# Kernel optimization log

Measured on AMD Instinct MI355X. Metric: run time of the kernel, lower is better.

## Reference

```python
import jax, jax.numpy as jnp
import numpy as np

DIMS = [2048, 1024, 512, 256, 128, 64, 32, 16, 8, 4, 2]
IN_CH = [3, 8, 32, 64, 64, 64, 128, 256, 512, 512, 512]
FEAT = [8, 32, 64, 64, 64, 128, 256, 512, 512, 512, 1024]
B = 512
K = 16


def setup_inputs() -> dict:
    key = jax.random.key(0)
    keys = jax.random.split(key, 64)
    inp = {"x": jax.random.normal(keys[0], (B, 3, 2048), dtype=jnp.float32)}
    for i, d in enumerate(DIMS):
        inp[f"c{i}"] = jax.random.randint(keys[1 + i], (d,), 0, 3, dtype=jnp.int64)
    for i in range(11):
        cin, f = IN_CH[i], FEAT[i]
        inp[f"W{i+1}"] = jax.random.normal(keys[20 + 2 * i], (3 * f, cin), dtype=jnp.float32) / jnp.sqrt(jnp.float32(cin))
        inp[f"b{i+1}"] = jnp.zeros((3 * f,), dtype=jnp.float32)
    inp["Wfc"] = jax.random.normal(keys[60], (K, 1024), dtype=jnp.float32) / jnp.sqrt(jnp.float32(1024))
    inp["bfc"] = jnp.zeros((K,), dtype=jnp.float32)
    return inp


def _kdconv(x, W, b, sel, featdim, dim):
    # pointwise conv (kernel size 1) + relu: [B, in, dim] -> [B, 3*featdim, dim]
    y = jax.nn.relu(jnp.einsum('oi,bid->bod', W, x) + b[None, :, None])
    bsz = y.shape[0]
    # faithful to torch: view [B, featdim, 3*dim], then gather index d*3 + sel[d]
    y = y.reshape(bsz, featdim, 3 * dim)
    idx = sel + 3 * jnp.arange(dim, dtype=sel.dtype)
    y = jnp.take(y, idx, axis=2)                       # [B, featdim, dim]
    y = y.reshape(bsz, featdim, dim // 2, 2)
    return jnp.max(y, axis=-1)                          # [B, featdim, dim//2]


def reference(x, c0, c1, c2, c3, c4, c5, c6, c7, c8, c9, c10,
              W1, b1, W2, b2, W3, b3, W4, b4, W5, b5, W6, b6,
              W7, b7, W8, b8, W9, b9, W10, b10, W11, b11, Wfc, bfc):
    cs = [c0, c1, c2, c3, c4, c5, c6, c7, c8, c9, c10]
    Ws = [W1, W2, W3, W4, W5, W6, W7, W8, W9, W10, W11]
    bs = [b1, b2, b3, b4, b5, b6, b7, b8, b9, b10, b11]
    y = x
    for i in range(11):
        y = _kdconv(y, Ws[i], bs[i], cs[i], FEAT[i], DIMS[i])
    y = y.reshape(-1, 1024)
    logits = y @ Wfc.T + bfc
    return jax.nn.log_softmax(logits, axis=1)
```

## Files before the change

### kernel.cpp

```cpp
#include <hip/hip_runtime.h>
#include <cstdint>
#include <cmath>


typedef __attribute__((ext_vector_type(8))) short bhalf8;
typedef __attribute__((ext_vector_type(4))) float floatx4;

__device__ __forceinline__ unsigned short f2bf(float f) {
    uint32_t u = __float_as_uint(f);
    u += 0x7FFFu + ((u >> 16) & 1u);
    return (unsigned short)(u >> 16);
}
__device__ __forceinline__ float bf2f(unsigned short u) {
    return __uint_as_float(((uint32_t)u) << 16);
}

struct WPrep {
    const float* src[9];
    unsigned short* dst[9];
    int n4[9];
};

__global__ __launch_bounds__(256)
void l01_kernel(const float* __restrict__ x,
                const float* __restrict__ W0, const float* __restrict__ b0,
                const int* __restrict__ sel0,
                const float* __restrict__ W1, const float* __restrict__ b1,
                const int* __restrict__ sel1,
                unsigned short* __restrict__ out,
                WPrep wp, int nL1) {
    const int tid = threadIdx.x;

    if ((int)blockIdx.x >= nL1) {
        const int stride = (gridDim.x - nL1) * 256;
        const int g0 = (blockIdx.x - nL1) * 256 + tid;
        #pragma unroll
        for (int l = 0; l < 9; ++l) {
            const float4* s = reinterpret_cast<const float4*>(wp.src[l]);
            uint2* d = reinterpret_cast<uint2*>(wp.dst[l]);
            for (int i = g0; i < wp.n4[l]; i += stride) {
                const float4 v = s[i];
                uint2 o;
                o.x = (uint32_t)f2bf(v.x) | ((uint32_t)f2bf(v.y) << 16);
                o.y = (uint32_t)f2bf(v.z) | ((uint32_t)f2bf(v.w) << 16);
                d[i] = o;
            }
        }
        return;
    }

    __shared__ float W0s[24][3]; __shared__ float b0s[24];
    __shared__ float W1s[96][8]; __shared__ float b1s[96];
    if (tid < 24) {
        W0s[tid][0] = W0[tid * 3 + 0];
        W0s[tid][1] = W0[tid * 3 + 1];
        W0s[tid][2] = W0[tid * 3 + 2];
        b0s[tid] = b0[tid];
    }
    if (tid < 96) {
        #pragma unroll
        for (int k = 0; k < 8; ++k) W1s[tid][k] = W1[tid * 8 + k];
        b1s[tid] = b1[tid];
    }
    __syncthreads();

    const int gid = blockIdx.x * 256 + tid;
    const int b  = gid >> 9;
    const int j1 = gid & 511;
    const float* xb = x + (size_t)b * 3 * 2048;

    float cols[2][8];
    int q1v[2];
    #pragma unroll
    for (int pos1 = 0; pos1 < 2; ++pos1) {
        const int d1 = 2 * j1 + pos1;
        const int e1 = 3 * d1 + sel1[d1];
        const int q1 = (e1 >= 1024) + (e1 >= 2048);
        const int p1 = e1 - q1 * 1024;
        q1v[pos1] = q1;

        float xv[2][3]; int qq0[2];
        #pragma unroll
        for (int pos0 = 0; pos0 < 2; ++pos0) {
            const int d0 = 2 * p1 + pos0;
            const int e0 = 3 * d0 + sel0[d0];
            const int q0 = (e0 >= 2048) + (e0 >= 4096);
            const int p0 = e0 - q0 * 2048;
            qq0[pos0] = q0;
            xv[pos0][0] = xb[p0];
            xv[pos0][1] = xb[2048 + p0];
            xv[pos0][2] = xb[4096 + p0];
        }
        #pragma unroll
        for (int f = 0; f < 8; ++f) {
            const int r0 = 3 * f + qq0[0], r1 = 3 * f + qq0[1];
            const float v0 = b0s[r0] + W0s[r0][0]*xv[0][0] + W0s[r0][1]*xv[0][1] + W0s[r0][2]*xv[0][2];
            const float v1 = b0s[r1] + W0s[r1][0]*xv[1][0] + W0s[r1][1]*xv[1][1] + W0s[r1][2]*xv[1][2];
            cols[pos1][f] = fmaxf(fmaxf(v0, v1), 0.f);
        }
    }

    unsigned short o[32];
    #pragma unroll
    for (int f = 0; f < 32; ++f) {
        const int r0 = 3 * f + q1v[0], r1 = 3 * f + q1v[1];
        float v0 = b1s[r0], v1 = b1s[r1];
        #pragma unroll
        for (int k = 0; k < 8; ++k) {
            v0 = fmaf(cols[0][k], W1s[r0][k], v0);
            v1 = fmaf(cols[1][k], W1s[r1][k], v1);
        }
        o[f] = f2bf(fmaxf(fmaxf(v0, v1), 0.f));
    }
    bhalf8* op = reinterpret_cast<bhalf8*>(out + (size_t)gid * 32);
    #pragma unroll
    for (int i = 0; i < 4; ++i) {
        bhalf8 v;
        #pragma unroll
        for (int k = 0; k < 8; ++k) v[k] = (short)o[8*i + k];
        op[i] = v;
    }
}

template<int CIN, int BT>
__global__ __launch_bounds__(256)
void kdmfma_kernel(const unsigned short* __restrict__ act,
                   const unsigned short* __restrict__ Wq,
                   const float* __restrict__ bias,
                   const int*   __restrict__ sel,
                   unsigned short* __restrict__ out,
                   int feat, int dim, int nbt) {
    constexpr int KS  = (CIN >= 128) ? 128 : CIN;
    constexpr int NH  = KS / 32;
    constexpr int LDK = KS + 8;
    constexpr int TPA = 256 / BT;
    constexpr int EA  = KS / TPA;
    constexpr int NSA = EA / 8;
    constexpr int NSW = KS / 32;
    constexpr int MF  = 2;
    constexpr int NF  = (BT == 64) ? 2 : 1;
    __shared__ __align__(16) unsigned short Ab[BT][LDK];
    __shared__ __align__(16) unsigned short Wb[64][LDK];

    const int dimh = dim >> 1;
    const int bt = blockIdx.x % nbt;
    const int j  = blockIdx.x / nbt;
    const int f0 = blockIdx.y * 64;
    const int b0 = bt * BT;

    const int tid  = threadIdx.x;
    const int lane = tid & 63;
    const int wave = tid >> 6;

    const int srowA = tid / TPA;
    const int kgA   = (tid % TPA) * EA;
    const int srowW = tid >> 2;
    const int kgW   = (tid & 3) * (KS / 4);

    const int rowBase = (BT == 64) ? (wave & 1) * 32 : 0;
    const int colBase = (BT == 64) ? (wave >> 1) * 32 : wave * 16;

    floatx4 acc[2][MF][NF];
    #pragma unroll
    for (int pp = 0; pp < 2; ++pp)
        #pragma unroll
        for (int mi = 0; mi < MF; ++mi)
            #pragma unroll
            for (int ni = 0; ni < NF; ++ni)
                acc[pp][mi][ni] = (floatx4){0.f, 0.f, 0.f, 0.f};
    int qv[2];

    #pragma unroll
    for (int pp = 0; pp < 2; ++pp) {
        const int d = 2 * j + pp;
        const int s = sel[d];
        const int e = 3 * d + s;
        const int q = (e >= dim) + (e >= 2 * dim);
        const int p = e - q * dim;
        qv[pp] = q;

        const unsigned short* Ap = act + ((size_t)(b0 + srowA) * dim + p) * CIN + kgA;
        const unsigned short* Wp = Wq + ((size_t)(3 * (f0 + srowW) + q)) * CIN + kgW;

        bhalf8 pa[NSA], pw[NSW];
        #pragma unroll
        for (int u = 0; u < NSA; ++u)
            pa[u] = *reinterpret_cast<const bhalf8*>(Ap + u * 8);
        #pragma unroll
        for (int u = 0; u < NSW; ++u)
            pw[u] = *reinterpret_cast<const bhalf8*>(Wp + u * 8);

        for (int k0 = 0; k0 < CIN; k0 += KS) {
            __syncthreads();
            #pragma unroll
            for (int u = 0; u < NSA; ++u)
                *reinterpret_cast<bhalf8*>(&Ab[srowA][kgA + u * 8]) = pa[u];
            #pragma unroll
            for (int u = 0; u < NSW; ++u)
                *reinterpret_cast<bhalf8*>(&Wb[srowW][kgW + u * 8]) = pw[u];
            if (k0 + KS < CIN) {
                #pragma unroll
                for (int u = 0; u < NSA; ++u)
                    pa[u] = *reinterpret_cast<const bhalf8*>(Ap + k0 + KS + u * 8);
                #pragma unroll
                for (int u = 0; u < NSW; ++u)
                    pw[u] = *reinterpret_cast<const bhalf8*>(Wp + k0 + KS + u * 8);
            }
            __syncthreads();

            #pragma unroll
            for (int ks = 0; ks < NH; ++ks) {
                const int kk = ks * 32 + (lane >> 4) * 8;
                bhalf8 aF[MF], bF[NF];
                #pragma unroll
                for (int mi = 0; mi < MF; ++mi)
                    aF[mi] = *reinterpret_cast<const bhalf8*>(
                        &Ab[rowBase + mi * 16 + (lane & 15)][kk]);
                #pragma unroll
                for (int ni = 0; ni < NF; ++ni)
                    bF[ni] = *reinterpret_cast<const bhalf8*>(
                        &Wb[colBase + ni * 16 + (lane & 15)][kk]);
                #pragma unroll
                for (int mi = 0; mi < MF; ++mi)
                    #pragma unroll
                    for (int ni = 0; ni < NF; ++ni)
                        acc[pp][mi][ni] = __builtin_amdgcn_mfma_f32_16x16x32_bf16(
                            aF[mi], bF[ni], acc[pp][mi][ni], 0, 0, 0);
            }
        }
    }

    const int orow = (lane >> 4) << 2;
    const int ocol = lane & 15;
    #pragma unroll
    for (int mi = 0; mi < MF; ++mi)
        #pragma unroll
        for (int ni = 0; ni < NF; ++ni) {
            const int fc = f0 + colBase + ni * 16 + ocol;
            const float bv0 = bias[3 * fc + qv[0]];
            const float bv1 = bias[3 * fc + qv[1]];
            #pragma unroll
            for (int i = 0; i < 4; ++i) {
                const int br = b0 + rowBase + mi * 16 + orow + i;
                const float v = fmaxf(fmaxf(acc[0][mi][ni][i] + bv0,
                                            acc[1][mi][ni][i] + bv1), 0.f);
                out[((size_t)br * dimh + j) * feat + fc] = f2bf(v);
            }
        }
}

__global__ __launch_bounds__(256)
void fc_lsm_kernel(const unsigned short* __restrict__ y,
                   const float* __restrict__ Wfc,
                   const float* __restrict__ bfc,
                   float* __restrict__ out) {
    const int b   = blockIdx.x;
    const int tid = threadIdx.x;
    __shared__ __align__(16) float ys[1024];
    __shared__ float lg[16];

    {
        const ushort4 v = reinterpret_cast<const ushort4*>(y + (size_t)b * 1024)[tid];
        ys[tid * 4 + 0] = bf2f(v.x);
        ys[tid * 4 + 1] = bf2f(v.y);
        ys[tid * 4 + 2] = bf2f(v.z);
        ys[tid * 4 + 3] = bf2f(v.w);
    }
    __syncthreads();

    const int l = tid >> 4, lane = tid & 15;
    const float4* w4 = reinterpret_cast<const float4*>(Wfc + (size_t)l * 1024);
    const float4* y4 = reinterpret_cast<const float4*>(ys);
    float p = 0.f;
    #pragma unroll
    for (int i = 0; i < 16; ++i) {
        const float4 a = y4[lane + 16 * i];
        const float4 w = w4[lane + 16 * i];
        p += a.x * w.x + a.y * w.y + a.z * w.z + a.w * w.w;
    }
    #pragma unroll
    for (int off = 8; off > 0; off >>= 1) p += __shfl_down(p, off, 16);
    if (lane == 0) lg[l] = p + bfc[l];
    __syncthreads();

    if (tid < 16) {
        float m = -1e30f;
        #pragma unroll
        for (int i = 0; i < 16; ++i) m = fmaxf(m, lg[i]);
        float s = 0.f;
        #pragma unroll
        for (int i = 0; i < 16; ++i) s += expf(lg[i] - m);
        out[b * 16 + tid] = lg[tid] - m - logf(s);
    }
}

extern "C" void kernel_launch(void* const* d_in, const int* in_sizes, int n_in,
                              void* d_out, int out_size, void* d_ws, size_t ws_size,
                              hipStream_t stream) {
    static const int LFEAT[11] = {8, 32, 64, 64, 64, 128, 256, 512, 512, 512, 1024};
    static const int LDIM[11]  = {2048, 1024, 512, 256, 128, 64, 32, 16, 8, 4, 2};
    static const int LCIN[11]  = {3, 8, 32, 64, 64, 64, 128, 256, 512, 512, 512};

    const float* x = (const float*)d_in[0];
    const int B = in_sizes[0] / (3 * 2048);

    const size_t slot = (size_t)B * 32 * 512;
    float* bufA = (float*)d_ws;
    float* bufB = bufA + slot;
    unsigned short* wq = (unsigned short*)(bufB + slot);

    const float* W[11]; const float* bi[11]; const int* sl[11];
    for (int i = 0; i < 11; ++i) {
        W[i]  = (const float*)d_in[12 + 2 * i];
        bi[i] = (const float*)d_in[13 + 2 * i];
        sl[i] = (const int*)d_in[1 + i];
    }

    unsigned short* wqp[11];
    {
        size_t off = 0;
        for (int i = 2; i <= 10; ++i) {
            wqp[i] = wq + off;
            off += (size_t)3 * LFEAT[i] * LCIN[i];
        }
    }

    unsigned short* actA = (unsigned short*)bufA;
    unsigned short* actB = (unsigned short*)bufB;

    {
        WPrep wp;
        for (int i = 2; i <= 10; ++i) {
            wp.src[i - 2] = W[i];
            wp.dst[i - 2] = wqp[i];
            wp.n4[i - 2]  = (3 * LFEAT[i] * LCIN[i]) / 4;
        }
        const int nL1 = (B * 512) / 256;
        l01_kernel<<<nL1 + 768, 256, 0, stream>>>(x, W[0], bi[0], sl[0],
                                                  W[1], bi[1], sl[1],
                                                  actB, wp, nL1);
    }

    const int nbt64 = B / 64;
    const int nbt32 = B / 32;

    {   dim3 g((LDIM[2]/2) * nbt64, LFEAT[2]/64);
        kdmfma_kernel<32,  64><<<g, 256, 0, stream>>>(actB, wqp[2], bi[2], sl[2], actA, LFEAT[2], LDIM[2], nbt64); }
    {   dim3 g((LDIM[3]/2) * nbt64, LFEAT[3]/64);
        kdmfma_kernel<64,  64><<<g, 256, 0, stream>>>(actA, wqp[3], bi[3], sl[3], actB, LFEAT[3], LDIM[3], nbt64); }
    {   dim3 g((LDIM[4]/2) * nbt64, LFEAT[4]/64);
        kdmfma_kernel<64,  64><<<g, 256, 0, stream>>>(actB, wqp[4], bi[4], sl[4], actA, LFEAT[4], LDIM[4], nbt64); }
    {   dim3 g((LDIM[5]/2) * nbt64, LFEAT[5]/64);
        kdmfma_kernel<64,  64><<<g, 256, 0, stream>>>(actA, wqp[5], bi[5], sl[5], actB, LFEAT[5], LDIM[5], nbt64); }
    {   dim3 g((LDIM[6]/2) * nbt64, LFEAT[6]/64);
        kdmfma_kernel<128, 64><<<g, 256, 0, stream>>>(actB, wqp[6], bi[6], sl[6], actA, LFEAT[6], LDIM[6], nbt64); }
    {   dim3 g((LDIM[7]/2) * nbt64, LFEAT[7]/64);
        kdmfma_kernel<256, 64><<<g, 256, 0, stream>>>(actA, wqp[7], bi[7], sl[7], actB, LFEAT[7], LDIM[7], nbt64); }

    {   dim3 g((LDIM[8]/2) * nbt32, LFEAT[8]/64);
        kdmfma_kernel<512, 32><<<g, 256, 0, stream>>>(actB, wqp[8], bi[8], sl[8], actA, LFEAT[8], LDIM[8], nbt32); }
    {   dim3 g((LDIM[9]/2) * nbt32, LFEAT[9]/64);
        kdmfma_kernel<512, 32><<<g, 256, 0, stream>>>(actA, wqp[9], bi[9], sl[9], actB, LFEAT[9], LDIM[9], nbt32); }
    {   dim3 g((LDIM[10]/2) * nbt32, LFEAT[10]/64);
        kdmfma_kernel<512, 32><<<g, 256, 0, stream>>>(actB, wqp[10], bi[10], sl[10], actA, LFEAT[10], LDIM[10], nbt32); }

    fc_lsm_kernel<<<B, 256, 0, stream>>>(actA, (const float*)d_in[34],
                                         (const float*)d_in[35], (float*)d_out);
}
```

Measured before the change: 99.37 us.

## Fuse layers 2-5 into one per-sample kernel keeping activations in LDS

Replaces four separate MFMA layer launches (layers 2-5) with a single chain_kernel where each block handles one batch sample and keeps intermediate activations in a swizzled LDS pool. Each block converts the fp32 weights for those layers to bf16 on the fly in shared memory, so the global bf16 weight-prep for those layers is dropped. This removes the global-memory round trips and launch overheads between layers. In exchange it uses about 78KB of LDS per block, which limits occupancy, and every block redundantly converts the weights.

```diff
diff --git a/kernel.cpp b/kernel.cpp
--- a/kernel.cpp
+++ b/kernel.cpp
@@ -35,7 +35,7 @@
         const int stride = (gridDim.x - nL1) * 256;
         const int g0 = (blockIdx.x - nL1) * 256 + tid;
         #pragma unroll
-        for (int l = 0; l < 9; ++l) {
+        for (int l = 0; l < 5; ++l) {
             const float4* s = reinterpret_cast<const float4*>(wp.src[l]);
             uint2* d = reinterpret_cast<uint2*>(wp.dst[l]);
             for (int i = g0; i < wp.n4[l]; i += stride) {
@@ -119,6 +119,130 @@
         #pragma unroll
         for (int k = 0; k < 8; ++k) v[k] = (short)o[8*i + k];
         op[i] = v;
+    }
+}
+
+
+template<int RB>
+__device__ __forceinline__ int swaddr(int row, int colbyte) {
+    constexpr int SM = (RB / 16 >= 8) ? 7 : (RB / 16 - 1);
+    return row * RB + (colbyte ^ ((row & SM) << 4));
+}
+
+template<int DIM, int CIN, int FEAT>
+__device__ __forceinline__ void kdlayer(char* pool, int offIn, int offOut,
+                                        int offW, int offMisc,
+                                        const float* __restrict__ Wg,
+                                        const float* __restrict__ bg,
+                                        const int* __restrict__ sel, int tid) {
+    constexpr int NH  = CIN / 32;
+    constexpr int MT  = DIM / 16;
+    constexpr int NT  = FEAT / 16;
+    constexpr int RBW = CIN * 2;
+    constexpr int RBO = FEAT * 2;
+    float* biasS = (float*)(pool + offMisc);
+    unsigned short* qp = (unsigned short*)(pool + offMisc + 3 * FEAT * 4);
+
+    {
+        constexpr int NW4 = 3 * FEAT * CIN / 4;
+        const float4* Ws = (const float4*)Wg;
+        for (int i = tid; i < NW4; i += 256) {
+            const float4 v = Ws[i];
+            const int row = (i * 4) / CIN, col = (i * 4) % CIN;
+            uint2 o;
+            o.x = (uint32_t)f2bf(v.x) | ((uint32_t)f2bf(v.y) << 16);
+            o.y = (uint32_t)f2bf(v.z) | ((uint32_t)f2bf(v.w) << 16);
+            *(uint2*)(pool + offW + swaddr<RBW>(row, col * 2)) = o;
+        }
+    }
+    for (int i = tid; i < 3 * FEAT; i += 256) biasS[i] = bg[i];
+    for (int d = tid; d < DIM; d += 256) {
+        const int e = 3 * d + sel[d];
+        const int q = (e >= DIM) + (e >= 2 * DIM);
+        qp[d] = (unsigned short)((q << 12) | (e - q * DIM));
+    }
+    __syncthreads();
+
+    const int lane = tid & 63, wave = tid >> 6;
+    const int g = lane >> 4, l15 = lane & 15;
+    for (int mt = wave; mt < MT; mt += 4) {
+        const int pa = qp[mt * 16 + l15] & 0xFFF;
+        bhalf8 aF[NH];
+        #pragma unroll
+        for (int ks = 0; ks < NH; ++ks)
+            aF[ks] = *(const bhalf8*)(pool + offIn +
+                        swaddr<RBW>(pa, (ks * 32 + g * 8) * 2));
+        const int r0 = mt * 16 + g * 4;
+        int qv[4];
+        #pragma unroll
+        for (int i = 0; i < 4; ++i) qv[i] = qp[r0 + i] >> 12;
+        const int j0 = mt * 8 + g * 2;
+        #pragma unroll
+        for (int nt = 0; nt < NT; ++nt) {
+            const int f = nt * 16 + l15;
+            floatx4 acc[3];
+            #pragma unroll
+            for (int q = 0; q < 3; ++q) acc[q] = (floatx4){0.f, 0.f, 0.f, 0.f};
+            #pragma unroll
+            for (int q = 0; q < 3; ++q)
+                #pragma unroll
+                for (int ks = 0; ks < NH; ++ks) {
+                    const bhalf8 bF = *(const bhalf8*)(pool + offW +
+                        swaddr<RBW>(3 * f + q, (ks * 32 + g * 8) * 2));
+                    acc[q] = __builtin_amdgcn_mfma_f32_16x16x32_bf16(
+                        aF[ks], bF, acc[q], 0, 0, 0);
+                }
+            float v[4];
+            #pragma unroll
+            for (int i = 0; i < 4; ++i) {
+                const float a0 = acc[0][i], a1 = acc[1][i], a2 = acc[2][i];
+                const int qi = qv[i];
+                const float pre = (qi == 0) ? a0 : (qi == 1 ? a1 : a2);
+                v[i] = pre + biasS[3 * f + qi];
+            }
+            *(unsigned short*)(pool + offOut + swaddr<RBO>(j0, f * 2)) =
+                f2bf(fmaxf(fmaxf(v[0], v[1]), 0.f));
+            *(unsigned short*)(pool + offOut + swaddr<RBO>(j0 + 1, f * 2)) =
+                f2bf(fmaxf(fmaxf(v[2], v[3]), 0.f));
+        }
+    }
+    __syncthreads();
+}
+
+__global__ __launch_bounds__(256)
+void chain_kernel(const unsigned short* __restrict__ act,
+                  unsigned short* __restrict__ out,
+                  const float* __restrict__ W2, const float* __restrict__ b2, const int* __restrict__ s2,
+                  const float* __restrict__ W3, const float* __restrict__ b3, const int* __restrict__ s3,
+                  const float* __restrict__ W4, const float* __restrict__ b4, const int* __restrict__ s4,
+                  const float* __restrict__ W5, const float* __restrict__ b5, const int* __restrict__ s5) {
+    __shared__ __align__(16) char pool[79872];
+    const int tid = threadIdx.x;
+    const int b = blockIdx.x;
+
+    {
+        const char* src = (const char*)(act + (size_t)b * 512 * 32);
+        #pragma unroll
+        for (int k = 0; k < 8; ++k) {
+            const int off = tid * 16 + k * 4096;
+            const bhalf8 v = *(const bhalf8*)(src + off);
+            *(bhalf8*)(pool + swaddr<64>(off >> 6, off & 63)) = v;
+        }
+    }
+
+    kdlayer<512, 32,  64>(pool, 0,     47104, 32768, 45056, W2, b2, s2, tid);
+    kdlayer<256, 64,  64>(pool, 47104, 0,     16384, 40960, W3, b3, s3, tid);
+    kdlayer<128, 64,  64>(pool, 0,     16384, 24576, 49152, W4, b4, s4, tid);
+    kdlayer< 64, 64, 128>(pool, 16384, 0,     24576, 73728, W5, b5, s5, tid);
+
+    {
+        char* dst = (char*)(out + (size_t)b * 32 * 128);
+        #pragma unroll
+        for (int k = 0; k < 2; ++k) {
+            const int off = tid * 16 + k * 4096;
+            const bhalf8 v = *(const bhalf8*)(pool + swaddr<256>(off >> 8, off & 255));
+            *(bhalf8*)(dst + off) = v;
+        }
     }
 }
 
@@ -319,7 +443,7 @@
     unsigned short* wqp[11];
     {
         size_t off = 0;
-        for (int i = 2; i <= 10; ++i) {
+        for (int i = 6; i <= 10; ++i) {
             wqp[i] = wq + off;
             off += (size_t)3 * LFEAT[i] * LCIN[i];
         }
@@ -330,40 +454,39 @@
 
     {
         WPrep wp;
-        for (int i = 2; i <= 10; ++i) {
-            wp.src[i - 2] = W[i];
-            wp.dst[i - 2] = wqp[i];
-            wp.n4[i - 2]  = (3 * LFEAT[i] * LCIN[i]) / 4;
-        }
+        for (int i = 6; i <= 10; ++i) {
+            wp.src[i - 6] = W[i];
+            wp.dst[i - 6] = wqp[i];
+            wp.n4[i - 6]  = (3 * LFEAT[i] * LCIN[i]) / 4;
+        }
+        for (int l = 5; l < 9; ++l) { wp.src[l] = nullptr; wp.dst[l] = nullptr; wp.n4[l] = 0; }
         const int nL1 = (B * 512) / 256;
         l01_kernel<<<nL1 + 768, 256, 0, stream>>>(x, W[0], bi[0], sl[0],
                                                   W[1], bi[1], sl[1],
                                                   actB, wp, nL1);
     }
 
+    chain_kernel<<<B, 256, 0, stream>>>(actB, actA,
+                                        W[2], bi[2], sl[2],
+                                        W[3], bi[3], sl[3],
+                                        W[4], bi[4], sl[4],
+                                        W[5], bi[5], sl[5]);
+
     const int nbt64 = B / 64;
     const int nbt32 = B / 32;
 
-    {   dim3 g((LDIM[2]/2) * nbt64, LFEAT[2]/64);
-        kdmfma_kernel<32,  64><<<g, 256, 0, stream>>>(actB, wqp[2], bi[2], sl[2], actA, LFEAT[2], LDIM[2], nbt64); }
-    {   dim3 g((LDIM[3]/2) * nbt64, LFEAT[3]/64);
-        kdmfma_kernel<64,  64><<<g, 256, 0, stream>>>(actA, wqp[3], bi[3], sl[3], actB, LFEAT[3], LDIM[3], nbt64); }
-    {   dim3 g((LDIM[4]/2) * nbt64, LFEAT[4]/64);
-        kdmfma_kernel<64,  64><<<g, 256, 0, stream>>>(actB, wqp[4], bi[4], sl[4], actA, LFEAT[4], LDIM[4], nbt64); }
-    {   dim3 g((LDIM[5]/2) * nbt64, LFEAT[5]/64);
-        kdmfma_kernel<64,  64><<<g, 256, 0, stream>>>(actA, wqp[5], bi[5], sl[5], actB, LFEAT[5], LDIM[5], nbt64); }
     {   dim3 g((LDIM[6]/2) * nbt64, LFEAT[6]/64);
-        kdmfma_kernel<128, 64><<<g, 256, 0, stream>>>(actB, wqp[6], bi[6], sl[6], actA, LFEAT[6], LDIM[6], nbt64); }
+        kdmfma_kernel<128, 64><<<g, 256, 0, stream>>>(actA, wqp[6], bi[6], sl[6], actB, LFEAT[6], LDIM[6], nbt64); }
     {   dim3 g((LDIM[7]/2) * nbt64, LFEAT[7]/64);
-        kdmfma_kernel<256, 64><<<g, 256, 0, stream>>>(actA, wqp[7], bi[7], sl[7], actB, LFEAT[7], LDIM[7], nbt64); }
+        kdmfma_kernel<256, 64><<<g, 256, 0, stream>>>(actB, wqp[7], bi[7], sl[7], actA, LFEAT[7], LDIM[7], nbt64); }
 
     {   dim3 g((LDIM[8]/2) * nbt32, LFEAT[8]/64);
-        kdmfma_kernel<512, 32><<<g, 256, 0, stream>>>(actB, wqp[8], bi[8], sl[8], actA, LFEAT[8], LDIM[8], nbt32); }
+        kdmfma_kernel<512, 32><<<g, 256, 0, stream>>>(actA, wqp[8], bi[8], sl[8], actB, LFEAT[8], LDIM[8], nbt32); }
     {   dim3 g((LDIM[9]/2) * nbt32, LFEAT[9]/64);
-        kdmfma_kernel<512, 32><<<g, 256, 0, stream>>>(actA, wqp[9], bi[9], sl[9], actB, LFEAT[9], LDIM[9], nbt32); }
+        kdmfma_kernel<512, 32><<<g, 256, 0, stream>>>(actB, wqp[9], bi[9], sl[9], actA, LFEAT[9], LDIM[9], nbt32); }
     {   dim3 g((LDIM[10]/2) * nbt32, LFEAT[10]/64);
-        kdmfma_kernel<512, 32><<<g, 256, 0, stream>>>(actB, wqp[10], bi[10], sl[10], actA, LFEAT[10], LDIM[10], nbt32); }
-
-    fc_lsm_kernel<<<B, 256, 0, stream>>>(actA, (const float*)d_in[34],
+        kdmfma_kernel<512, 32><<<g, 256, 0, stream>>>(actA, wqp[10], bi[10], sl[10], actB, LFEAT[10], LDIM[10], nbt32); }
+
+    fc_lsm_kernel<<<B, 256, 0, stream>>>(actB, (const float*)d_in[34],
                                          (const float*)d_in[35], (float*)d_out);
 }
```

Measured after the change: 102.3 us. 1.03x slower.
